# Performance work log

Hardware: AMD Instinct MI355X
Metric: run time of the kernel (lower is better)

The kernel has to match this reference:

```python
import jax, jax.numpy as jnp
import numpy as np

H = 16          # hidden_size
L = 24          # num_layers
LEN_TRAIN = 96
LEN_PRED = 48
B = 256         # leading dim of input (acts as TIME axis for the LSTMs, see notes)


def setup_inputs() -> dict:
    key = jax.random.key(0)
    ks = jax.random.split(key, 16)
    s = 1.0 / np.sqrt(H)  # PyTorch LSTM/Linear init scale
    u = lambda k, shp: jax.random.uniform(k, shp, jnp.float32, -s, s)
    return {
        "x": jax.random.normal(ks[0], (B, 1, LEN_TRAIN), jnp.float32),
        # lstm1: layer0 input_size=1, layers 1..23 input_size=2H
        "W_ih0_1": u(ks[1], (2, 4 * H, 1)),
        "W_ih_1": u(ks[2], (L - 1, 2, 4 * H, 2 * H)),
        "W_hh_1": u(ks[3], (L, 2, 4 * H, H)),
        "b_ih_1": u(ks[4], (L, 2, 4 * H)),
        "b_hh_1": u(ks[5], (L, 2, 4 * H)),
        # lstm2: all layers input_size=2H
        "W_ih_2": u(ks[6], (L, 2, 4 * H, 2 * H)),
        "W_hh_2": u(ks[7], (L, 2, 4 * H, H)),
        "b_ih_2": u(ks[8], (L, 2, 4 * H)),
        "b_hh_2": u(ks[9], (L, 2, 4 * H)),
        "fc1_w": u(ks[10], (1000, 2 * LEN_PRED * H)),
        "fc1_b": u(ks[11], (1000,)),
        "fc2_w": u(ks[12], (LEN_PRED, 1000)),
        "fc2_b": u(ks[13], (LEN_PRED,)),
    }


def _lstm_dir(x, Wih, Whh, bih, bhh, reverse):
    # x: (T, N, in). Precompute input-gate GEMM over whole sequence.
    xg = jnp.einsum("tni,gi->tng", x, Wih) + bih + bhh  # (T, N, 4H)

    def step(carry, g_in):
        h, c = carry
        g = g_in + h @ Whh.T
        i, f, gg, o = jnp.split(g, 4, axis=-1)  # PyTorch gate order i,f,g,o
        c = jax.nn.sigmoid(f) * c + jax.nn.sigmoid(i) * jnp.tanh(gg)
        h = jax.nn.sigmoid(o) * jnp.tanh(c)
        return (h, c), h

    N = x.shape[1]
    init = (jnp.zeros((N, H), x.dtype), jnp.zeros((N, H), x.dtype))
    _, hs = jax.lax.scan(step, init, xg, reverse=reverse)
    return hs  # (T, N, H), in original time order


def _bilstm_stack(x, Wih_per_layer, Whh, bih, bhh):
    for l in range(Whh.shape[0]):
        Wih = Wih_per_layer[l]
        fwd = _lstm_dir(x, Wih[0], Whh[l, 0], bih[l, 0], bhh[l, 0], False)
        bwd = _lstm_dir(x, Wih[1], Whh[l, 1], bih[l, 1], bhh[l, 1], True)
        x = jnp.concatenate([fwd, bwd], axis=-1)  # (T, N, 2H)
    return x


def reference(x, W_ih0_1, W_ih_1, W_hh_1, b_ih_1, b_hh_1,
              W_ih_2, W_hh_2, b_ih_2, b_hh_2,
              fc1_w, fc1_b, fc2_w, fc2_b):
    xp = jnp.transpose(x, (0, 2, 1))  # (B, 96, 1); dim0 is the LSTM time axis (batch_first=False quirk)
    wih1 = [W_ih0_1] + [W_ih_1[i] for i in range(L - 1)]
    h = _bilstm_stack(xp, wih1, W_hh_1, b_ih_1, b_hh_1)      # (B, 96, 2H)
    x1 = h[:, -LEN_PRED:, :]                                  # (B, 48, 2H)
    wih2 = [W_ih_2[i] for i in range(L)]
    h2 = _bilstm_stack(x1, wih2, W_hh_2, b_ih_2, b_hh_2)      # (B, 48, 2H)
    z = h2 + x1
    flat = z.reshape(z.shape[0], -1)                          # (B, 1536)
    y = jax.nn.relu(flat @ fc1_w.T + fc1_b) @ fc2_w.T + fc2_b # (B, 48)
    return jnp.transpose(y.reshape(y.shape[0], LEN_PRED, 1), (0, 2, 1))  # (B, 1, 48)
```

## Files before the change

### kernel.cpp

```cpp
#include <hip/hip_runtime.h>


template <int SEL>
__device__ __forceinline__ float quad_bcast(float v) {
  return __int_as_float(__builtin_amdgcn_update_dpp(
      0, __float_as_int(v), SEL * 0x55, 0xF, 0xF, true));
}

template <int IN_SZ, int N>
__global__ __launch_bounds__(256) void lstm_layer(
    const float* __restrict__ xin, float* __restrict__ xout,
    const float* __restrict__ Wih, const float* __restrict__ Whh,
    const float* __restrict__ bih, const float* __restrict__ bhh,
    int t_stride, int n_off) {
  __shared__ float xg[256 * 64];

  const int tid = threadIdx.x;
  const int lane = tid & 63;
  const int w = tid >> 6;
  const int d = blockIdx.x / N;
  const int n = blockIdx.x % N;

  {
    const int r = lane;
    const float bias = bih[d * 64 + r] + bhh[d * 64 + r];
    if constexpr (IN_SZ == 1) {
      const float wih0 = Wih[d * 64 + r];
      for (int ti = 0; ti < 64; ++ti) {
        const int t = w * 64 + ti;
        const float xv = xin[(size_t)t * t_stride + (n + n_off)];
        xg[t * 64 + r] = fmaf(wih0, xv, bias);
      }
    } else {
      float wih[IN_SZ];
#pragma unroll
      for (int k = 0; k < IN_SZ; ++k)
        wih[k] = Wih[(size_t)(d * 64 + r) * IN_SZ + k];
      for (int ti = 0; ti < 64; ++ti) {
        const int t = w * 64 + ti;
        const float4* p4 = reinterpret_cast<const float4*>(
            xin + (size_t)t * t_stride + (size_t)(n + n_off) * IN_SZ);
        float a0 = bias, a1 = 0.f, a2 = 0.f, a3 = 0.f;
#pragma unroll
        for (int q = 0; q < IN_SZ / 4; ++q) {
          const float4 xv = p4[q];
          a0 = fmaf(wih[4 * q + 0], xv.x, a0);
          a1 = fmaf(wih[4 * q + 1], xv.y, a1);
          a2 = fmaf(wih[4 * q + 2], xv.z, a2);
          a3 = fmaf(wih[4 * q + 3], xv.w, a3);
        }
        xg[t * 64 + r] = (a0 + a1) + (a2 + a3);
      }
    }
  }
  __syncthreads();
  if (w != 0) return;

  const int j = lane >> 2;
  const int g = lane & 3;
  const int r = g * 16 + j;

  float whh[16];
#pragma unroll
  for (int k = 0; k < 16; ++k) whh[k] = Whh[(d * 64 + r) * 16 + k];

  const float s_ = (g == 2) ? 2.885390082f : -1.442695041f;
  const float m_ = (g == 2) ? -2.0f : 1.0f;
  const float b_ = (g == 2) ? 1.0f : 0.0f;

  float hs[16];
#pragma unroll
  for (int k = 0; k < 16; ++k) hs[k] = 0.f;
  float c = 0.f;

  const int dt = d ? -1 : 1;
  int t = d ? 255 : 0;
  float cur = xg[t * 64 + r];
  float* outp = xout + ((size_t)t * N + n) * 32 + d * 16 + j;
  const ptrdiff_t ostep = (ptrdiff_t)dt * N * 32;

  for (int tt = 0; tt < 256; ++tt) {
    const int tn = (t + dt) & 255;
    const float nxt = xg[tn * 64 + r];

    float a0 = cur, a1 = 0.f, a2 = 0.f, a3 = 0.f;
#pragma unroll
    for (int k = 0; k < 16; k += 4) {
      a0 = fmaf(whh[k + 0], hs[k + 0], a0);
      a1 = fmaf(whh[k + 1], hs[k + 1], a1);
      a2 = fmaf(whh[k + 2], hs[k + 2], a2);
      a3 = fmaf(whh[k + 3], hs[k + 3], a3);
    }
    const float gv = (a0 + a1) + (a2 + a3);

    const float e = __builtin_amdgcn_exp2f(s_ * gv);
    const float v = fmaf(m_, __builtin_amdgcn_rcpf(1.0f + e), b_);
    const float si = quad_bcast<0>(v);
    const float sf = quad_bcast<1>(v);
    const float tg = quad_bcast<2>(v);
    const float so = quad_bcast<3>(v);

    c = fmaf(sf, c, si * tg);
    const float e2 = __builtin_amdgcn_exp2f(2.885390082f * c);
    const float th = fmaf(-2.0f, __builtin_amdgcn_rcpf(1.0f + e2), 1.0f);
    const float h = so * th;

    if (g == 0) *outp = h;
    outp += ostep;

    const int hb = __float_as_int(h);
#pragma unroll
    for (int k = 0; k < 16; ++k)
      hs[k] = __int_as_float(__builtin_amdgcn_readlane(hb, 4 * k));

    cur = nxt;
    t += dt;
  }
}

__global__ __launch_bounds__(256) void fc1_kernel(
    const float* __restrict__ h2,
    const float* __restrict__ x1b,
    const float* __restrict__ w1, const float* __restrict__ b1,
    float* __restrict__ y1) {
  __shared__ float Zs[16][68];
  __shared__ float Ws[16][68];
  const int tid = threadIdx.x;
  const int m0 = blockIdx.x * 64;
  const int b0 = blockIdx.y * 64;
  const int rr = tid >> 2;
  const int c4 = (tid & 3) * 4;
  const int tx = tid & 15, ty = tid >> 4;

  float acc[4][4];
#pragma unroll
  for (int i = 0; i < 4; ++i)
#pragma unroll
    for (int jj = 0; jj < 4; ++jj) acc[i][jj] = 0.f;

  const bool wvalid = (m0 + rr) < 1000;

  for (int k0 = 0; k0 < 1536; k0 += 16) {
    const int k = k0 + c4;
    const float4 za =
        *reinterpret_cast<const float4*>(h2 + (size_t)(b0 + rr) * 1536 + k);
    const float4 zb = *reinterpret_cast<const float4*>(
        x1b + (size_t)(b0 + rr) * 3072 + 1536 + k);
    Zs[c4 + 0][rr] = za.x + zb.x;
    Zs[c4 + 1][rr] = za.y + zb.y;
    Zs[c4 + 2][rr] = za.z + zb.z;
    Zs[c4 + 3][rr] = za.w + zb.w;
    float4 wv = make_float4(0.f, 0.f, 0.f, 0.f);
    if (wvalid)
      wv = *reinterpret_cast<const float4*>(w1 + (size_t)(m0 + rr) * 1536 + k);
    Ws[c4 + 0][rr] = wv.x;
    Ws[c4 + 1][rr] = wv.y;
    Ws[c4 + 2][rr] = wv.z;
    Ws[c4 + 3][rr] = wv.w;
    __syncthreads();
#pragma unroll
    for (int kk = 0; kk < 16; ++kk) {
      const float4 av = *reinterpret_cast<const float4*>(&Zs[kk][ty * 4]);
      const float4 bv = *reinterpret_cast<const float4*>(&Ws[kk][tx * 4]);
      const float a_[4] = {av.x, av.y, av.z, av.w};
      const float b_[4] = {bv.x, bv.y, bv.z, bv.w};
#pragma unroll
      for (int i = 0; i < 4; ++i)
#pragma unroll
        for (int jj = 0; jj < 4; ++jj)
          acc[i][jj] = fmaf(a_[i], b_[jj], acc[i][jj]);
    }
    __syncthreads();
  }
#pragma unroll
  for (int i = 0; i < 4; ++i) {
    const int b = b0 + ty * 4 + i;
#pragma unroll
    for (int jj = 0; jj < 4; ++jj) {
      const int m = m0 + tx * 4 + jj;
      if (m < 1000) {
        float v = acc[i][jj] + b1[m];
        y1[(size_t)b * 1000 + m] = v > 0.f ? v : 0.f;
      }
    }
  }
}

__global__ __launch_bounds__(64) void fc2_kernel(
    const float* __restrict__ y1, const float* __restrict__ w2,
    const float* __restrict__ b2, float* __restrict__ out) {
  __shared__ float ys[1000];
  const int b = blockIdx.x;
  for (int k = threadIdx.x; k < 1000; k += 64) ys[k] = y1[(size_t)b * 1000 + k];
  __syncthreads();
  const int p = threadIdx.x;
  if (p < 48) {
    float a0 = b2[p], a1 = 0.f, a2 = 0.f, a3 = 0.f;
    const float* wr = w2 + (size_t)p * 1000;
    for (int k = 0; k < 1000; k += 4) {
      const float4 wv = *reinterpret_cast<const float4*>(wr + k);
      a0 = fmaf(ys[k + 0], wv.x, a0);
      a1 = fmaf(ys[k + 1], wv.y, a1);
      a2 = fmaf(ys[k + 2], wv.z, a2);
      a3 = fmaf(ys[k + 3], wv.w, a3);
    }
    out[(size_t)b * 48 + p] = (a0 + a1) + (a2 + a3);
  }
}

extern "C" void kernel_launch(void* const* d_in, const int* in_sizes, int n_in,
                              void* d_out, int out_size, void* d_ws,
                              size_t ws_size, hipStream_t stream) {
  const float* x = (const float*)d_in[0];
  const float* W_ih0_1 = (const float*)d_in[1];
  const float* W_ih_1 = (const float*)d_in[2];
  const float* W_hh_1 = (const float*)d_in[3];
  const float* b_ih_1 = (const float*)d_in[4];
  const float* b_hh_1 = (const float*)d_in[5];
  const float* W_ih_2 = (const float*)d_in[6];
  const float* W_hh_2 = (const float*)d_in[7];
  const float* b_ih_2 = (const float*)d_in[8];
  const float* b_hh_2 = (const float*)d_in[9];
  const float* fc1_w = (const float*)d_in[10];
  const float* fc1_b = (const float*)d_in[11];
  const float* fc2_w = (const float*)d_in[12];
  const float* fc2_b = (const float*)d_in[13];

  float* ws = (float*)d_ws;
  float* buf0 = ws;
  float* buf1 = ws + 786432;
  float* y1 = ws + 2 * 786432;
  float* q0 = buf0;
  float* q1 = buf0 + 393216;

  lstm_layer<1, 96><<<192, 256, 0, stream>>>(x, buf0, W_ih0_1, W_hh_1, b_ih_1,
                                             b_hh_1, 96, 0);
  for (int l = 1; l < 24; ++l) {
    const float* in = (l & 1) ? buf0 : buf1;
    float* outb = (l & 1) ? buf1 : buf0;
    lstm_layer<32, 96><<<192, 256, 0, stream>>>(
        in, outb, W_ih_1 + (size_t)(l - 1) * 4096, W_hh_1 + (size_t)l * 2048,
        b_ih_1 + l * 128, b_hh_1 + l * 128, 3072, 0);
  }
  lstm_layer<32, 48><<<96, 256, 0, stream>>>(buf1, q0, W_ih_2, W_hh_2, b_ih_2,
                                             b_hh_2, 3072, 48);
  for (int l = 1; l < 24; ++l) {
    const float* in = (l & 1) ? q0 : q1;
    float* outb = (l & 1) ? q1 : q0;
    lstm_layer<32, 48><<<96, 256, 0, stream>>>(
        in, outb, W_ih_2 + (size_t)l * 4096, W_hh_2 + (size_t)l * 2048,
        b_ih_2 + l * 128, b_hh_2 + l * 128, 1536, 0);
  }
  fc1_kernel<<<dim3(16, 4), 256, 0, stream>>>(q1, buf1, fc1_w, fc1_b, y1);
  fc2_kernel<<<256, 64, 0, stream>>>(y1, fc2_w, fc2_b, (float*)d_out);
}
```

Before: 2.640 ms.

## Stage LSTM inputs and outputs through LDS with coalesced loads and stores

The input-projection phase now loads each time step's 32-float row cooperatively with coalesced float4 loads into shared memory (layer 0 uses one load plus readlane broadcasts), then computes gates from LDS. The recurrent loop writes h into the xg buffer instead of issuing scattered global stores every step, and after a barrier all 256 threads write the outputs with float4 stores. The recurrence is also unrolled by two, and fc1 software-prefetches the next tile into registers. This removes strided global traffic from the serial critical path, at the cost of an extra barrier and reusing xg, which is only safe because slot t has already been consumed when it is overwritten.

Result: faster. 2.241 ms (-15.1%).

```diff
diff --git a/kernel.cpp b/kernel.cpp
--- a/kernel.cpp
+++ b/kernel.cpp
@@ -25,25 +25,47 @@
     const int r = lane;
     const float bias = bih[d * 64 + r] + bhh[d * 64 + r];
     if constexpr (IN_SZ == 1) {
+      const float xv =
+          xin[(size_t)(w * 64 + lane) * t_stride + (n + n_off)];
       const float wih0 = Wih[d * 64 + r];
+      const int xvb = __float_as_int(xv);
+      for (int ti = 0; ti < 64; ++ti) {
+        const float xs = __int_as_float(__builtin_amdgcn_readlane(xvb, ti));
+        xg[(w * 64 + ti) * 64 + r] = fmaf(wih0, xs, bias);
+      }
+    } else {
+      const int r8 = lane >> 3;
+      const int c = lane & 7;
+      const float* gbase = xin + (size_t)(n + n_off) * 32 + c * 4;
+      float4 v[8];
+#pragma unroll
+      for (int i = 0; i < 8; ++i) {
+        const int t = w * 64 + i * 8 + r8;
+        v[i] = *reinterpret_cast<const float4*>(gbase + (size_t)t * t_stride);
+      }
+#pragma unroll
+      for (int i = 0; i < 8; ++i) {
+        const int t = w * 64 + i * 8 + r8;
+        *reinterpret_cast<float4*>(&xg[t * 64 + 32 + c * 4]) = v[i];
+      }
+      float wih[32];
+      const float4* wp =
+          reinterpret_cast<const float4*>(Wih + (size_t)(d * 64 + r) * 32);
+#pragma unroll
+      for (int q = 0; q < 8; ++q) {
+        const float4 t4 = wp[q];
+        wih[4 * q + 0] = t4.x;
+        wih[4 * q + 1] = t4.y;
+        wih[4 * q + 2] = t4.z;
+        wih[4 * q + 3] = t4.w;
+      }
       for (int ti = 0; ti < 64; ++ti) {
         const int t = w * 64 + ti;
-        const float xv = xin[(size_t)t * t_stride + (n + n_off)];
-        xg[t * 64 + r] = fmaf(wih0, xv, bias);
-      }
-    } else {
-      float wih[IN_SZ];
-#pragma unroll
-      for (int k = 0; k < IN_SZ; ++k)
-        wih[k] = Wih[(size_t)(d * 64 + r) * IN_SZ + k];
-      for (int ti = 0; ti < 64; ++ti) {
-        const int t = w * 64 + ti;
-        const float4* p4 = reinterpret_cast<const float4*>(
-            xin + (size_t)t * t_stride + (size_t)(n + n_off) * IN_SZ);
+        const float4* xr = reinterpret_cast<const float4*>(&xg[t * 64 + 32]);
         float a0 = bias, a1 = 0.f, a2 = 0.f, a3 = 0.f;
 #pragma unroll
-        for (int q = 0; q < IN_SZ / 4; ++q) {
-          const float4 xv = p4[q];
+        for (int q = 0; q < 8; ++q) {
+          const float4 xv = xr[q];
           a0 = fmaf(wih[4 * q + 0], xv.x, a0);
           a1 = fmaf(wih[4 * q + 1], xv.y, a1);
           a2 = fmaf(wih[4 * q + 2], xv.z, a2);
@@ -54,67 +76,83 @@
     }
   }
   __syncthreads();
-  if (w != 0) return;
-
-  const int j = lane >> 2;
-  const int g = lane & 3;
-  const int r = g * 16 + j;
-
-  float whh[16];
-#pragma unroll
-  for (int k = 0; k < 16; ++k) whh[k] = Whh[(d * 64 + r) * 16 + k];
-
-  const float s_ = (g == 2) ? 2.885390082f : -1.442695041f;
-  const float m_ = (g == 2) ? -2.0f : 1.0f;
-  const float b_ = (g == 2) ? 1.0f : 0.0f;
-
-  float hs[16];
-#pragma unroll
-  for (int k = 0; k < 16; ++k) hs[k] = 0.f;
-  float c = 0.f;
-
-  const int dt = d ? -1 : 1;
-  int t = d ? 255 : 0;
-  float cur = xg[t * 64 + r];
-  float* outp = xout + ((size_t)t * N + n) * 32 + d * 16 + j;
-  const ptrdiff_t ostep = (ptrdiff_t)dt * N * 32;
-
-  for (int tt = 0; tt < 256; ++tt) {
-    const int tn = (t + dt) & 255;
-    const float nxt = xg[tn * 64 + r];
-
-    float a0 = cur, a1 = 0.f, a2 = 0.f, a3 = 0.f;
-#pragma unroll
-    for (int k = 0; k < 16; k += 4) {
-      a0 = fmaf(whh[k + 0], hs[k + 0], a0);
-      a1 = fmaf(whh[k + 1], hs[k + 1], a1);
-      a2 = fmaf(whh[k + 2], hs[k + 2], a2);
-      a3 = fmaf(whh[k + 3], hs[k + 3], a3);
-    }
-    const float gv = (a0 + a1) + (a2 + a3);
-
-    const float e = __builtin_amdgcn_exp2f(s_ * gv);
-    const float v = fmaf(m_, __builtin_amdgcn_rcpf(1.0f + e), b_);
-    const float si = quad_bcast<0>(v);
-    const float sf = quad_bcast<1>(v);
-    const float tg = quad_bcast<2>(v);
-    const float so = quad_bcast<3>(v);
-
-    c = fmaf(sf, c, si * tg);
-    const float e2 = __builtin_amdgcn_exp2f(2.885390082f * c);
-    const float th = fmaf(-2.0f, __builtin_amdgcn_rcpf(1.0f + e2), 1.0f);
-    const float h = so * th;
-
-    if (g == 0) *outp = h;
-    outp += ostep;
-
-    const int hb = __float_as_int(h);
-#pragma unroll
-    for (int k = 0; k < 16; ++k)
-      hs[k] = __int_as_float(__builtin_amdgcn_readlane(hb, 4 * k));
-
-    cur = nxt;
-    t += dt;
+
+  if (w == 0) {
+    const int j = lane >> 2;
+    const int g = lane & 3;
+    const int r = g * 16 + j;
+
+    float whh[16];
+#pragma unroll
+    for (int k = 0; k < 16; ++k) whh[k] = Whh[(d * 64 + r) * 16 + k];
+
+    const float s_ = (g == 2) ? 2.885390082f : -1.442695041f;
+    const float m_ = (g == 2) ? -2.0f : 1.0f;
+    const float b_ = (g == 2) ? 1.0f : 0.0f;
+
+    float hs[16];
+#pragma unroll
+    for (int k = 0; k < 16; ++k) hs[k] = 0.f;
+    float c = 0.f;
+
+    const int dt = d ? -1 : 1;
+    int t = d ? 255 : 0;
+    float cur0 = xg[t * 64 + r];
+    float cur1 = xg[(t + dt) * 64 + r];
+
+#define LSTM_STEP(CUR, TT)                                              \
+  {                                                                     \
+    float a0 = (CUR), a1 = 0.f, a2 = 0.f, a3 = 0.f;                     \
+    _Pragma("unroll") for (int k = 0; k < 16; k += 4) {                 \
+      a0 = fmaf(whh[k + 0], hs[k + 0], a0);                             \
+      a1 = fmaf(whh[k + 1], hs[k + 1], a1);                             \
+      a2 = fmaf(whh[k + 2], hs[k + 2], a2);                             \
+      a3 = fmaf(whh[k + 3], hs[k + 3], a3);                             \
+    }                                                                   \
+    const float gv = (a0 + a1) + (a2 + a3);                             \
+    const float e = __builtin_amdgcn_exp2f(s_ * gv);                    \
+    const float v = fmaf(m_, __builtin_amdgcn_rcpf(1.0f + e), b_);      \
+    const float si = quad_bcast<0>(v);                                  \
+    const float sf = quad_bcast<1>(v);                                  \
+    const float tg = quad_bcast<2>(v);                                  \
+    const float so = quad_bcast<3>(v);                                  \
+    c = fmaf(sf, c, si * tg);                                           \
+    const float e2 = __builtin_amdgcn_exp2f(2.885390082f * c);          \
+    const float th = fmaf(-2.0f, __builtin_amdgcn_rcpf(1.0f + e2), 1.0f); \
+    const float h = so * th;                                            \
+    xg[(TT)*64 + lane] = h;    \
+    const int hb = __float_as_int(h);                                   \
+    _Pragma("unroll") for (int k = 0; k < 16; ++k) hs[k] =              \
+        __int_as_float(__builtin_amdgcn_readlane(hb, 4 * k));           \
+  }
+
+    for (int tt = 0; tt < 256; tt += 2) {
+      const float nx0 = xg[((t + 2 * dt) & 255) * 64 + r];
+      LSTM_STEP(cur0, t)
+      const float nx1 = xg[((t + 3 * dt) & 255) * 64 + r];
+      LSTM_STEP(cur1, t + dt)
+      cur0 = nx0;
+      cur1 = nx1;
+      t += 2 * dt;
+    }
+#undef LSTM_STEP
+  }
+  __syncthreads();
+
+  {
+    const int q4 = tid & 3;
+    const int tb = tid >> 2;
+#pragma unroll
+    for (int p = 0; p < 4; ++p) {
+      const int t = p * 64 + tb;
+      float4 v;
+      v.x = xg[t * 64 + 16 * q4 + 0];
+      v.y = xg[t * 64 + 16 * q4 + 4];
+      v.z = xg[t * 64 + 16 * q4 + 8];
+      v.w = xg[t * 64 + 16 * q4 + 12];
+      *reinterpret_cast<float4*>(xout + ((size_t)t * N + n) * 32 + d * 16 +
+                                 q4 * 4) = v;
+    }
   }
 }
 
@@ -139,24 +177,29 @@
     for (int jj = 0; jj < 4; ++jj) acc[i][jj] = 0.f;
 
   const bool wvalid = (m0 + rr) < 1000;
+  const float* zr = h2 + (size_t)(b0 + rr) * 1536 + c4;
+  const float* zr2 = x1b + (size_t)(b0 + rr) * 3072 + 1536 + c4;
+  const float* wr = w1 + (size_t)(m0 + rr) * 1536 + c4;
+
+  float4 za = *reinterpret_cast<const float4*>(zr);
+  float4 zb = *reinterpret_cast<const float4*>(zr2);
+  float4 wv = wvalid ? *reinterpret_cast<const float4*>(wr)
+                     : make_float4(0.f, 0.f, 0.f, 0.f);
 
   for (int k0 = 0; k0 < 1536; k0 += 16) {
-    const int k = k0 + c4;
-    const float4 za =
-        *reinterpret_cast<const float4*>(h2 + (size_t)(b0 + rr) * 1536 + k);
-    const float4 zb = *reinterpret_cast<const float4*>(
-        x1b + (size_t)(b0 + rr) * 3072 + 1536 + k);
     Zs[c4 + 0][rr] = za.x + zb.x;
     Zs[c4 + 1][rr] = za.y + zb.y;
     Zs[c4 + 2][rr] = za.z + zb.z;
     Zs[c4 + 3][rr] = za.w + zb.w;
-    float4 wv = make_float4(0.f, 0.f, 0.f, 0.f);
-    if (wvalid)
-      wv = *reinterpret_cast<const float4*>(w1 + (size_t)(m0 + rr) * 1536 + k);
     Ws[c4 + 0][rr] = wv.x;
     Ws[c4 + 1][rr] = wv.y;
     Ws[c4 + 2][rr] = wv.z;
     Ws[c4 + 3][rr] = wv.w;
+    if (k0 + 16 < 1536) {
+      za = *reinterpret_cast<const float4*>(zr + k0 + 16);
+      zb = *reinterpret_cast<const float4*>(zr2 + k0 + 16);
+      if (wvalid) wv = *reinterpret_cast<const float4*>(wr + k0 + 16);
+    }
     __syncthreads();
 #pragma unroll
     for (int kk = 0; kk < 16; ++kk) {
@@ -179,8 +222,8 @@
     for (int jj = 0; jj < 4; ++jj) {
       const int m = m0 + tx * 4 + jj;
       if (m < 1000) {
-        float v = acc[i][jj] + b1[m];
-        y1[(size_t)b * 1000 + m] = v > 0.f ? v : 0.f;
+        float vo = acc[i][jj] + b1[m];
+        y1[(size_t)b * 1000 + m] = vo > 0.f ? vo : 0.f;
       }
     }
   }
```
